# Kernel optimization log

Measured on AMD Instinct MI355X. Metric: run time of the kernel, lower is better.

Reference implementation:

```python
import jax, jax.numpy as jnp
import numpy as np

B, S, DIM = 2, 2048, 2048
QH, KVH = 32, 8
HD = DIM // QH            # 64
KV_DIM = HD * KVH         # 512
MAX_LEN = 2048
SCALE = HD ** -0.5
NEG_INF = -1e30


def _rope_cache(seq_len, head_dim, max_len, theta=10000.0, factor=8.0):
    # faithful to generate_sin_cos_pos_emb (causal branch, offset=0),
    # cache built at max_len then sliced to seq_len by the caller
    idx = np.arange(0, head_dim, 2, dtype=np.float64) / head_dim
    inv_freq = 1.0 / theta ** idx
    if factor > 1.0:
        seq_eff = max(max_len, max_len)  # generate called with seq_len=max_length
        adj = (factor * seq_eff / max_len - (factor - 1.0)) ** (head_dim / (head_dim - 2.0))
        inv_freq = 1.0 / (theta * adj) ** idx
    pos = np.arange(0, max_len, dtype=np.float64)
    freqs = np.einsum('i,j->ij', pos, inv_freq)
    emb = np.concatenate([freqs, freqs], axis=-1)  # [max_len, head_dim]
    cos = jnp.asarray(np.cos(emb)[:seq_len], dtype=jnp.float32)
    sin = jnp.asarray(np.sin(emb)[:seq_len], dtype=jnp.float32)
    return cos, sin


def _rotate_half(x):
    x1, x2 = jnp.split(x, 2, axis=-1)
    return jnp.concatenate([-x2, x1], axis=-1)


def _apply_rope(x, cos, sin):
    # x: [B, H, S, D]; cos/sin: [S, D]
    return x * cos + _rotate_half(x) * sin


def setup_inputs() -> dict:
    key = jax.random.key(0)
    ks = jax.random.split(key, 11)
    s = 0.02
    return {
        'query': jax.random.normal(ks[0], (B, S, DIM), jnp.float32),
        'key':   jax.random.normal(ks[1], (B, S, DIM), jnp.float32),
        'value': jax.random.normal(ks[2], (B, S, DIM), jnp.float32),
        'w_q': jax.random.normal(ks[3], (DIM, DIM), jnp.float32) * s,
        'b_q': jnp.zeros((DIM,), jnp.float32),
        'w_k': jax.random.normal(ks[4], (DIM, KV_DIM), jnp.float32) * s,
        'b_k': jnp.zeros((KV_DIM,), jnp.float32),
        'w_v': jax.random.normal(ks[5], (DIM, KV_DIM), jnp.float32) * s,
        'b_v': jnp.zeros((KV_DIM,), jnp.float32),
        'w_o': jax.random.normal(ks[6], (DIM, DIM), jnp.float32) * s,
        'b_o': jnp.zeros((DIM,), jnp.float32),
    }


def reference(query, key, value, w_q, b_q, w_k, b_k, w_v, b_v, w_o, b_o):
    # projections (weights stored as [in, out])
    q = query @ w_q + b_q                                    # [B,S,DIM]
    k = key   @ w_k + b_k                                    # [B,S,KV_DIM]
    v = value @ w_v + b_v                                    # [B,S,KV_DIM]

    q = q.reshape(B, S, QH, HD).transpose(0, 2, 1, 3)        # [B,QH,S,HD]
    k = k.reshape(B, S, KVH, HD).transpose(0, 2, 1, 3)       # [B,KVH,S,HD]
    v = v.reshape(B, S, KVH, HD).transpose(0, 2, 1, 3)       # [B,KVH,S,HD]

    cos, sin = _rope_cache(S, HD, MAX_LEN)
    q = _apply_rope(q, cos, sin)
    k = _apply_rope(k, cos, sin)

    # GQA: group queries per kv head (equivalent to repeat_interleave on K/V)
    G = QH // KVH
    qg = q.reshape(B, KVH, G, S, HD)
    scores = jnp.einsum('bhgqd,bhkd->bhgqk', qg, k) * SCALE  # [B,KVH,G,S,S]
    causal = jnp.tril(jnp.ones((S, S), dtype=bool))
    scores = jnp.where(causal, scores, NEG_INF)
    probs = jax.nn.softmax(scores, axis=-1)
    ctx = jnp.einsum('bhgqk,bhkd->bhgqd', probs, v)          # [B,KVH,G,S,HD]
    ctx = ctx.reshape(B, QH, S, HD).transpose(0, 2, 1, 3).reshape(B, S, DIM)
    return ctx @ w_o + b_o                                   # [B,S,DIM]
```

## Files before the change

kernel.cpp:

```cpp
#include <hip/hip_runtime.h>
#include <hip/hip_bf16.h>

typedef __hip_bfloat16 bf16_t;
typedef __attribute__((ext_vector_type(8))) short bf16x8;
typedef __attribute__((ext_vector_type(4))) float f32x4;

#define S_LEN   2048
#define D_MODEL 2048
#define N_QH    32
#define N_KVH   8
#define HEAD_D  64
#define KV_D    512
#define M_ROWS  4096
#define QK_SCALE (0.125f * 1.44269504088896340736f)
#define NQT     16

__global__ void rope_table_kernel(float* __restrict__ cosT, float* __restrict__ sinT) {
    int pos = blockIdx.x * 2 + (threadIdx.x >> 5);
    int j   = threadIdx.x & 31;
    double invf = pow(10000.0, -(double)(2 * j) / 64.0);
    double a = (double)pos * invf;
    cosT[pos * 32 + j] = (float)cos(a);
    sinT[pos * 32 + j] = (float)sin(a);
}

__global__ void wt_conv_all_kernel(const float* __restrict__ wq, const float* __restrict__ wk,
                                   const float* __restrict__ wv, const float* __restrict__ wo,
                                   bf16_t* __restrict__ tq, bf16_t* __restrict__ tk,
                                   bf16_t* __restrict__ tv, bf16_t* __restrict__ to) {
    __shared__ float tile[32][33];
    const int x = blockIdx.x;
    const float* W; bf16_t* Wt; int N, nb;
    if (x < 64)       { W = wq; Wt = tq; N = D_MODEL; nb = x; }
    else if (x < 80)  { W = wk; Wt = tk; N = KV_D;    nb = x - 64; }
    else if (x < 96)  { W = wv; Wt = tv; N = KV_D;    nb = x - 80; }
    else              { W = wo; Wt = to; N = D_MODEL; nb = x - 96; }
    const int K = D_MODEL;
    int n0 = nb * 32, k0 = blockIdx.y * 32;
    int tx = threadIdx.x & 31, ty = threadIdx.x >> 5;
#pragma unroll
    for (int i = 0; i < 4; i++) {
        int r = ty + i * 8;
        tile[r][tx] = W[(size_t)(k0 + r) * N + n0 + tx];
    }
    __syncthreads();
#pragma unroll
    for (int i = 0; i < 4; i++) {
        int r = ty + i * 8;
        Wt[(size_t)(n0 + r) * K + k0 + tx] = __float2bfloat16(tile[tx][r]);
    }
}

struct __align__(8) bf16x4s { bf16_t x, y, z, w; };

__device__ __forceinline__ void async_copy16(const bf16_t* g, bf16_t* l) {
    __builtin_amdgcn_global_load_lds((const __attribute__((address_space(1))) void*)g,
                                     (__attribute__((address_space(3))) void*)l, 16, 0, 0);
}

template <int ROPE, int OUTF32, int QSCALE>
__global__ __launch_bounds__(256, 2)
void gqa_gemm_kernel(const bf16_t* __restrict__ A, const bf16_t* __restrict__ Bt,
                     const float* __restrict__ bias, void* __restrict__ Cout,
                     int M, int N, int K,
                     const float* __restrict__ cosT, const float* __restrict__ sinT) {
    __shared__ __align__(16) bf16_t As[128 * 64];
    __shared__ __align__(16) bf16_t Bs[128 * 64];

    const int t = threadIdx.x;
    const int bx = blockIdx.x;
    const int xcd = bx & 7, j = bx >> 3;
    const int am0 = (((xcd >> 1) << 3) + (j >> 3)) * 128;
    const int bn0 = (((xcd & 1) << 3) + (j & 7)) * 128;

    const int l = t & 63, w = t >> 6;
    const int wr = w >> 1, wc = w & 1;
    const int lr = l & 15, lk = l >> 4;

    f32x4 acc[4][4];
#pragma unroll
    for (int i = 0; i < 4; i++)
#pragma unroll
        for (int jx = 0; jx < 4; jx++) acc[i][jx] = (f32x4)0.0f;

    const int r0 = t >> 3;
    const int c  = (t & 7) ^ (r0 & 7);
    const bf16_t* aptr = A + (size_t)(am0 + r0) * K + c * 8;
    const bf16_t* bptr = Bt + (size_t)(bn0 + r0) * K + c * 8;
    bf16_t* aLds = As + r0 * 64 + (t & 7) * 8;
    bf16_t* bLds = Bs + r0 * 64 + (t & 7) * 8;

    for (int k0 = 0; k0 < K; k0 += 64) {
#pragma unroll
        for (int s = 0; s < 4; ++s) {
            async_copy16(aptr + (size_t)(s * 32) * K + k0, aLds + s * 2048);
            async_copy16(bptr + (size_t)(s * 32) * K + k0, bLds + s * 2048);
        }
        __syncthreads();

        bf16x8 af[4][2], bfr[4][2];
#pragma unroll
        for (int mi = 0; mi < 4; mi++)
#pragma unroll
            for (int ks = 0; ks < 2; ks++)
                af[mi][ks] = *(const bf16x8*)&As[(wr * 64 + mi * 16 + lr) * 64 +
                                 ((ks * 32 + lk * 8) ^ ((lr & 7) << 3))];
#pragma unroll
        for (int ni = 0; ni < 4; ni++)
#pragma unroll
            for (int ks = 0; ks < 2; ks++)
                bfr[ni][ks] = *(const bf16x8*)&Bs[(wc * 64 + ni * 16 + lr) * 64 +
                                  ((ks * 32 + lk * 8) ^ ((lr & 7) << 3))];
#pragma unroll
        for (int mi = 0; mi < 4; mi++)
#pragma unroll
            for (int ni = 0; ni < 4; ni++)
#pragma unroll
                for (int ks = 0; ks < 2; ks++)
                    acc[mi][ni] = __builtin_amdgcn_mfma_f32_16x16x32_bf16(
                        af[mi][ks], bfr[ni][ks], acc[mi][ni], 0, 0, 0);
        __syncthreads();
    }

#pragma unroll
    for (int mi = 0; mi < 4; mi++) {
#pragma unroll
        for (int reg = 0; reg < 4; reg++) {
            int row = am0 + wr * 64 + mi * 16 + lk * 4 + reg;
            if (OUTF32) {
                float* out = (float*)Cout;
#pragma unroll
                for (int ni = 0; ni < 4; ni++) {
                    int col = bn0 + wc * 64 + ni * 16 + lr;
                    out[(size_t)row * N + col] = acc[mi][ni][reg] + bias[col];
                }
            } else if (ROPE) {
                bf16_t* out = (bf16_t*)Cout;
                int pos = row & (S_LEN - 1);
#pragma unroll
                for (int np = 0; np < 2; np++) {
                    int jj = np * 16 + lr;
                    float cs = cosT[pos * 32 + jj];
                    float sn = sinT[pos * 32 + jj];
                    int col1 = bn0 + wc * 64 + np * 16 + lr;
                    float x1 = acc[mi][np][reg] + bias[col1];
                    float x2 = acc[mi][np + 2][reg] + bias[col1 + 32];
                    float o1 = x1 * cs - x2 * sn;
                    float o2 = x2 * cs + x1 * sn;
                    if (QSCALE) { o1 *= QK_SCALE; o2 *= QK_SCALE; }
                    out[(size_t)row * N + col1]      = __float2bfloat16(o1);
                    out[(size_t)row * N + col1 + 32] = __float2bfloat16(o2);
                }
            } else {
                bf16_t* out = (bf16_t*)Cout;
#pragma unroll
                for (int ni = 0; ni < 4; ni++) {
                    int col = bn0 + wc * 64 + ni * 16 + lr;
                    out[(size_t)row * N + col] =
                        __float2bfloat16(acc[mi][ni][reg] + bias[col]);
                }
            }
        }
    }
}

__global__ __launch_bounds__(256, 4)
void gqa_kvc_kernel(const float* __restrict__ Key, const float* __restrict__ Val,
                    const float* __restrict__ Query,
                    const bf16_t* __restrict__ Wtk, const bf16_t* __restrict__ Wtv,
                    const float* __restrict__ bk, const float* __restrict__ bv,
                    bf16_t* __restrict__ Kout, bf16_t* __restrict__ VtOut,
                    bf16_t* __restrict__ Qbf,
                    const float* __restrict__ cosT, const float* __restrict__ sinT) {
    __shared__ __align__(16) char smem[9216];
    bf16_t* As  = (bf16_t*)smem;
    bf16_t* Bs  = (bf16_t*)(smem + 4096);
    bf16_t* VtE = (bf16_t*)smem;

    const int bx = blockIdx.x;
    const int t = threadIdx.x;

    if (bx >= 1024) {
        int tid = (bx - 1024) * 256 + t;
        const int total = M_ROWS * D_MODEL / 4;
#pragma unroll 4
        for (int i = tid; i < total; i += 512 * 256) {
            float4 v = ((const float4*)Query)[i];
            bf16x4s o;
            o.x = __float2bfloat16(v.x);
            o.y = __float2bfloat16(v.y);
            o.z = __float2bfloat16(v.z);
            o.w = __float2bfloat16(v.w);
            ((bf16x4s*)Qbf)[i] = o;
        }
        return;
    }

    constexpr int K = D_MODEL;
    const int xcd = bx & 7;
    const int j   = bx >> 3;
    const int z   = xcd >> 2;
    const int am0 = (((xcd & 3) << 4) + (j >> 3)) * 64;
    const int bn0 = (j & 7) * 64;

    const float* A32  = z ? Val : Key;
    const bf16_t* Bt  = z ? Wtv : Wtk;
    const float* bias = z ? bv : bk;

    const int l = t & 63, w = t >> 6;
    const int lr = l & 15, lk = l >> 4;

    f32x4 acc[4];
#pragma unroll
    for (int jx = 0; jx < 4; jx++) acc[jx] = (f32x4)0.0f;

    const int sr = t >> 2;
    const int sc = (t & 3) * 8;
    const float*  aptr = A32 + (size_t)(am0 + sr) * K + sc;
    const bf16_t* bptr = Bt + (size_t)(bn0 + sr) * K + sc;
    bf16_t* aLds = As + sr * 32 + sc;
    bf16_t* bLds = Bs + t * 8;

    float4 pa0 = ((const float4*)aptr)[0];
    float4 pa1 = ((const float4*)aptr)[1];

    for (int it = 0; it < K / 32; ++it) {
        union { bf16x8 v; bf16_t e[8]; } u;
        u.e[0] = __float2bfloat16(pa0.x); u.e[1] = __float2bfloat16(pa0.y);
        u.e[2] = __float2bfloat16(pa0.z); u.e[3] = __float2bfloat16(pa0.w);
        u.e[4] = __float2bfloat16(pa1.x); u.e[5] = __float2bfloat16(pa1.y);
        u.e[6] = __float2bfloat16(pa1.z); u.e[7] = __float2bfloat16(pa1.w);
        *(bf16x8*)aLds = u.v;
        async_copy16(bptr + it * 32, bLds);
        __builtin_amdgcn_sched_barrier(0);
        if (it + 1 < K / 32) {
            const float* ap = aptr + (it + 1) * 32;
            pa0 = ((const float4*)ap)[0];
            pa1 = ((const float4*)ap)[1];
            __builtin_amdgcn_sched_barrier(0);
            asm volatile("s_waitcnt lgkmcnt(0) vmcnt(2)" ::: "memory");
        } else {
            asm volatile("s_waitcnt lgkmcnt(0) vmcnt(0)" ::: "memory");
        }
        __builtin_amdgcn_sched_barrier(0);
        __builtin_amdgcn_s_barrier();
        __builtin_amdgcn_sched_barrier(0);

        bf16x8 af = *(const bf16x8*)&As[(w * 16 + lr) * 32 + lk * 8];
        bf16x8 bfr[4];
#pragma unroll
        for (int ni = 0; ni < 4; ni++)
            bfr[ni] = *(const bf16x8*)&Bs[(ni * 16 + lr) * 32 + lk * 8];
#pragma unroll
        for (int ni = 0; ni < 4; ni++)
            acc[ni] = __builtin_amdgcn_mfma_f32_16x16x32_bf16(af, bfr[ni], acc[ni], 0, 0, 0);
        __builtin_amdgcn_sched_barrier(0);
        __builtin_amdgcn_s_barrier();
        __builtin_amdgcn_sched_barrier(0);
    }

    if (z == 0) {
#pragma unroll
        for (int reg = 0; reg < 4; reg++) {
            int row = am0 + w * 16 + lk * 4 + reg;
            int pos = row & (S_LEN - 1);
#pragma unroll
            for (int np = 0; np < 2; np++) {
                int jj = np * 16 + lr;
                float cs = cosT[pos * 32 + jj];
                float sn = sinT[pos * 32 + jj];
                int col1 = bn0 + np * 16 + lr;
                float x1 = acc[np][reg] + bias[col1];
                float x2 = acc[np + 2][reg] + bias[col1 + 32];
                Kout[(size_t)row * KV_D + col1]      = __float2bfloat16(x1 * cs - x2 * sn);
                Kout[(size_t)row * KV_D + col1 + 32] = __float2bfloat16(x2 * cs + x1 * sn);
            }
        }
    } else {
        __syncthreads();
#pragma unroll
        for (int ni = 0; ni < 4; ni++) {
            bf16x4s pk;
            pk.x = __float2bfloat16(acc[ni][0] + bias[bn0 + ni * 16 + lr]);
            pk.y = __float2bfloat16(acc[ni][1] + bias[bn0 + ni * 16 + lr]);
            pk.z = __float2bfloat16(acc[ni][2] + bias[bn0 + ni * 16 + lr]);
            pk.w = __float2bfloat16(acc[ni][3] + bias[bn0 + ni * 16 + lr]);
            *(bf16x4s*)&VtE[(ni * 16 + lr) * 72 + w * 16 + lk * 4] = pk;
        }
        __syncthreads();
        const int d = t & 63, w2 = t >> 6;
        const int bI = am0 >> 11;
        const int kvhI = bn0 >> 6;
        const int sl = (am0 & (S_LEN - 1)) + w2 * 16;
        bf16_t* dst = VtOut + ((size_t)(bI * N_KVH + kvhI) * HEAD_D + d) * S_LEN + sl;
        const bf16_t* src = &VtE[d * 72 + w2 * 16];
        *(bf16x8*)dst       = *(const bf16x8*)src;
        *(bf16x8*)(dst + 8) = *(const bf16x8*)(src + 8);
    }
}

__device__ __forceinline__ void stage_K8(const bf16_t* KB, bf16_t* dst, int kt, int t) {
    const int skey = t >> 3;
    const int c    = (t & 7) ^ (skey & 7);
    async_copy16(KB + (size_t)(kt * 64 + skey) * KV_D + c * 8, dst + t * 8);
}
__device__ __forceinline__ void stage_V8(const bf16_t* VTb, bf16_t* dst, int kt, int t) {
    const int sd = t >> 3;
    const int c  = (t & 7) ^ (sd & 7);
    async_copy16(VTb + (size_t)sd * S_LEN + kt * 64 + c * 8, dst + t * 8);
}

__global__ __launch_bounds__(512, 4)
void gqa_attn_kernel(const bf16_t* __restrict__ Q, const bf16_t* __restrict__ Kb,
                     const bf16_t* __restrict__ VT, bf16_t* __restrict__ Ctx) {
    __shared__ __align__(16) bf16_t Ks[2][64 * 64];
    __shared__ __align__(16) bf16_t Vs[2][64 * 64];
    __shared__ __align__(16) bf16_t Pw[8][16 * 72];

    const int t = threadIdx.x, l = t & 63, w = t >> 6;
    const int lr = l & 15, lk = l >> 4;

    const int flat = blockIdx.x;
    const int xcd = flat & 7, j0 = flat >> 3;
    const int combo  = xcd * 2 + (j0 >> 5);
    const int within = j0 & 31;
    const int b   = combo >> 3;
    const int kvh = combo & 7;
    const int h   = kvh * 4 + (within >> 3);
    const int p   = within & 7;

    const bf16_t* KB  = Kb + (size_t)b * S_LEN * KV_D + kvh * HEAD_D;
    const bf16_t* VTb = VT + ((size_t)(b * N_KVH + kvh) * HEAD_D) * S_LEN;

#pragma unroll
    for (int half = 0; half < 2; ++half) {
        const int qt  = half ? (NQT - 1 - p) : p;
        const int q0w = qt * 128 + w * 16;
        const int qg  = q0w + lr;

        bf16x8 qf[2];
        {
            const bf16_t* qrow = Q + ((size_t)(b * S_LEN + qg)) * D_MODEL + h * HEAD_D;
            qf[0] = *(const bf16x8*)(qrow + lk * 8);
            qf[1] = *(const bf16x8*)(qrow + 32 + lk * 8);
        }

        float lrow = 0.f;
        f32x4 oaccT[4];
#pragma unroll
        for (int df = 0; df < 4; df++) oaccT[df] = (f32x4)0.0f;

        const int nkt = 2 * qt + 2;

        stage_K8(KB, Ks[0], 0, t);
        stage_V8(VTb, Vs[0], 0, t);
        __syncthreads();

        int cur = 0;
        for (int kt = 0; kt < nkt; ++kt) {
            const bool pre = (kt + 1 < nkt);
            if (pre) {
                stage_K8(KB, Ks[cur ^ 1], kt + 1, t);
                stage_V8(VTb, Vs[cur ^ 1], kt + 1, t);
            }

            if (kt * 64 <= q0w + 15) {
                const bool diag = (kt * 64 + 63 > q0w);

                f32x4 sfrT[4];
#pragma unroll
                for (int ni = 0; ni < 4; ni++) sfrT[ni] = (f32x4)0.0f;
                __builtin_amdgcn_s_setprio(1);
#pragma unroll
                for (int ni = 0; ni < 4; ni++)
#pragma unroll
                    for (int ks = 0; ks < 2; ks++) {
                        bf16x8 kf = *(const bf16x8*)&Ks[cur][(ni * 16 + lr) * 64 +
                                        ((ks * 32 + lk * 8) ^ ((lr & 7) << 3))];
                        sfrT[ni] = __builtin_amdgcn_mfma_f32_16x16x32_bf16(kf, qf[ks],
                                                                           sfrT[ni], 0, 0, 0);
                    }
                __builtin_amdgcn_s_setprio(0);

                float rsp[4] = {0.f, 0.f, 0.f, 0.f};
                float pe[16];
#pragma unroll
                for (int ni = 0; ni < 4; ni++)
#pragma unroll
                    for (int r = 0; r < 4; r++) {
                        float sc = sfrT[ni][r];
                        if (diag) {
                            int keyg = kt * 64 + ni * 16 + lk * 4 + r;
                            if (keyg > qg) sc = -1e30f;
                        }
                        float e = exp2f(sc);
                        pe[ni * 4 + r] = e;
                        rsp[ni] += e;
                    }
                float rs = (rsp[0] + rsp[1]) + (rsp[2] + rsp[3]);
                rs += __shfl_xor(rs, 16);
                rs += __shfl_xor(rs, 32);
                lrow += rs;

#pragma unroll
                for (int ni = 0; ni < 4; ni++) {
                    bf16x4s pk;
                    pk.x = __float2bfloat16(pe[ni * 4 + 0]);
                    pk.y = __float2bfloat16(pe[ni * 4 + 1]);
                    pk.z = __float2bfloat16(pe[ni * 4 + 2]);
                    pk.w = __float2bfloat16(pe[ni * 4 + 3]);
                    *(bf16x4s*)&Pw[w][lr * 72 + ni * 16 + lk * 4] = pk;
                }

                __builtin_amdgcn_s_setprio(1);
#pragma unroll
                for (int ks = 0; ks < 2; ks++) {
                    bf16x8 pf = *(const bf16x8*)&Pw[w][lr * 72 + ks * 32 + lk * 8];
#pragma unroll
                    for (int df = 0; df < 4; df++) {
                        bf16x8 vf = *(const bf16x8*)&Vs[cur][(df * 16 + lr) * 64 +
                                        ((ks * 32 + lk * 8) ^ ((lr & 7) << 3))];
                        oaccT[df] = __builtin_amdgcn_mfma_f32_16x16x32_bf16(vf, pf,
                                            oaccT[df], 0, 0, 0);
                    }
                }
                __builtin_amdgcn_s_setprio(0);
            }

            __syncthreads();
            cur ^= 1;
        }

        {
            float inv = 1.0f / lrow;
            bf16_t* crow = Ctx + ((size_t)(b * S_LEN + qg)) * D_MODEL + h * HEAD_D;
#pragma unroll
            for (int df = 0; df < 4; df++) {
                bf16x4s ov;
                ov.x = __float2bfloat16(oaccT[df][0] * inv);
                ov.y = __float2bfloat16(oaccT[df][1] * inv);
                ov.z = __float2bfloat16(oaccT[df][2] * inv);
                ov.w = __float2bfloat16(oaccT[df][3] * inv);
                *(bf16x4s*)(crow + df * 16 + lk * 4) = ov;
            }
        }
    }
}

extern "C" void kernel_launch(void* const* d_in, const int* in_sizes, int n_in,
                              void* d_out, int out_size, void* d_ws, size_t ws_size,
                              hipStream_t stream) {
    const float* query = (const float*)d_in[0];
    const float* key_  = (const float*)d_in[1];
    const float* value = (const float*)d_in[2];
    const float* w_q = (const float*)d_in[3];
    const float* b_q = (const float*)d_in[4];
    const float* w_k = (const float*)d_in[5];
    const float* b_k = (const float*)d_in[6];
    const float* w_v = (const float*)d_in[7];
    const float* b_v = (const float*)d_in[8];
    const float* w_o = (const float*)d_in[9];
    const float* b_o = (const float*)d_in[10];
    float* out = (float*)d_out;

    char* ws = (char*)d_ws;
    bf16_t* Abuf = (bf16_t*)(ws);
    bf16_t* qb   = (bf16_t*)(ws + (size_t)(16 << 20));
    bf16_t* kb   = (bf16_t*)(ws + (size_t)(32 << 20));
    bf16_t* vt   = (bf16_t*)(ws + (size_t)(36 << 20));
    bf16_t* wtq  = (bf16_t*)(ws + (size_t)(40 << 20));
    bf16_t* wtk  = (bf16_t*)(ws + (size_t)(48 << 20));
    bf16_t* wtv  = (bf16_t*)(ws + (size_t)(50 << 20));
    bf16_t* wto  = (bf16_t*)(ws + (size_t)(52 << 20));
    float* cosT  = (float*)(ws + (size_t)(60 << 20));
    float* sinT  = (float*)(ws + (size_t)(60 << 20) + (256 << 10));

    rope_table_kernel<<<S_LEN / 2, 64, 0, stream>>>(cosT, sinT);

    wt_conv_all_kernel<<<dim3(160, 64), 256, 0, stream>>>(w_q, w_k, w_v, w_o,
                                                          wtq, wtk, wtv, wto);

    gqa_kvc_kernel<<<1536, 256, 0, stream>>>(key_, value, query, wtk, wtv,
                                             b_k, b_v, kb, vt, Abuf, cosT, sinT);

    gqa_gemm_kernel<1, 0, 1><<<512, 256, 0, stream>>>(
        Abuf, wtq, b_q, qb, M_ROWS, D_MODEL, D_MODEL, cosT, sinT);

    gqa_attn_kernel<<<512, 512, 0, stream>>>(qb, kb, vt, Abuf);

    gqa_gemm_kernel<0, 1, 0><<<512, 256, 0, stream>>>(
        Abuf, wto, b_o, out, M_ROWS, D_MODEL, D_MODEL, cosT, sinT);
}
```

Before: 215.5 us.

## Fuse Q projection into KV projection kernel and compute softmax denominator via MFMA

The rope table generation moves into an extra block column of the weight-conversion kernel, and the Q projection GEMM (with bias, RoPE and scale) now runs in the same launch as the K/V projections. It reads fp32 query directly instead of first writing a bf16 copy. This removes two kernel launches and a full query conversion pass. In attention, the per-row exp sum is accumulated with an extra MFMA against a ones vector instead of shuffles, which trades a little matrix work for fewer VALU/shuffle ops. The Q path uses a 64x128 tile with one wave per 16 rows, which may lower its efficiency compared with the dedicated GEMM kernel.

```diff
diff --git a/kernel.cpp b/kernel.cpp
--- a/kernel.cpp
+++ b/kernel.cpp
@@ -15,21 +15,25 @@
 #define QK_SCALE (0.125f * 1.44269504088896340736f)
 #define NQT     16
 
-__global__ void rope_table_kernel(float* __restrict__ cosT, float* __restrict__ sinT) {
-    int pos = blockIdx.x * 2 + (threadIdx.x >> 5);
-    int j   = threadIdx.x & 31;
-    double invf = pow(10000.0, -(double)(2 * j) / 64.0);
-    double a = (double)pos * invf;
-    cosT[pos * 32 + j] = (float)cos(a);
-    sinT[pos * 32 + j] = (float)sin(a);
-}
-
 __global__ void wt_conv_all_kernel(const float* __restrict__ wq, const float* __restrict__ wk,
                                    const float* __restrict__ wv, const float* __restrict__ wo,
                                    bf16_t* __restrict__ tq, bf16_t* __restrict__ tk,
-                                   bf16_t* __restrict__ tv, bf16_t* __restrict__ to) {
+                                   bf16_t* __restrict__ tv, bf16_t* __restrict__ to,
+                                   float* __restrict__ cosT, float* __restrict__ sinT) {
+    const int x = blockIdx.x;
+    if (x == 160) {
+        int j = threadIdx.x & 31;
+        double invf = pow(10000.0, -(double)(2 * j) / 64.0);
+#pragma unroll
+        for (int i = 0; i < 4; i++) {
+            int pos = blockIdx.y * 32 + i * 8 + (threadIdx.x >> 5);
+            double a = (double)pos * invf;
+            cosT[pos * 32 + j] = (float)cos(a);
+            sinT[pos * 32 + j] = (float)sin(a);
+        }
+        return;
+    }
     __shared__ float tile[32][33];
-    const int x = blockIdx.x;
     const float* W; bf16_t* Wt; int N, nb;
     if (x < 64)       { W = wq; Wt = tq; N = D_MODEL; nb = x; }
     else if (x < 80)  { W = wk; Wt = tk; N = KV_D;    nb = x - 64; }
@@ -165,38 +169,104 @@
 }
 
 __global__ __launch_bounds__(256, 4)
-void gqa_kvc_kernel(const float* __restrict__ Key, const float* __restrict__ Val,
+void gqa_kvq_kernel(const float* __restrict__ Key, const float* __restrict__ Val,
                     const float* __restrict__ Query,
                     const bf16_t* __restrict__ Wtk, const bf16_t* __restrict__ Wtv,
+                    const bf16_t* __restrict__ Wtq,
                     const float* __restrict__ bk, const float* __restrict__ bv,
+                    const float* __restrict__ bq,
                     bf16_t* __restrict__ Kout, bf16_t* __restrict__ VtOut,
-                    bf16_t* __restrict__ Qbf,
+                    bf16_t* __restrict__ Qout,
                     const float* __restrict__ cosT, const float* __restrict__ sinT) {
-    __shared__ __align__(16) char smem[9216];
+    __shared__ __align__(16) char smem[12288];
     bf16_t* As  = (bf16_t*)smem;
     bf16_t* Bs  = (bf16_t*)(smem + 4096);
     bf16_t* VtE = (bf16_t*)smem;
 
     const int bx = blockIdx.x;
     const int t = threadIdx.x;
+    const int l = t & 63, w = t >> 6;
+    const int lr = l & 15, lk = l >> 4;
+    const int sr = t >> 2;
+    const int sc = (t & 3) * 8;
+    constexpr int K = D_MODEL;
 
     if (bx >= 1024) {
-        int tid = (bx - 1024) * 256 + t;
-        const int total = M_ROWS * D_MODEL / 4;
-#pragma unroll 4
-        for (int i = tid; i < total; i += 512 * 256) {
-            float4 v = ((const float4*)Query)[i];
-            bf16x4s o;
-            o.x = __float2bfloat16(v.x);
-            o.y = __float2bfloat16(v.y);
-            o.z = __float2bfloat16(v.z);
-            o.w = __float2bfloat16(v.w);
-            ((bf16x4s*)Qbf)[i] = o;
+        const int qbx = bx - 1024;
+        const int xcd = qbx & 7;
+        const int j   = qbx >> 3;
+        const int am0 = ((xcd << 3) + (j & 7)) * 64;
+        const int bn0 = (j >> 3) * 128;
+
+        f32x4 acc[8];
+#pragma unroll
+        for (int jx = 0; jx < 8; jx++) acc[jx] = (f32x4)0.0f;
+
+        const float*  aptr = Query + (size_t)(am0 + sr) * K + sc;
+        const bf16_t* bptr = Wtq + (size_t)(bn0 + sr) * K + sc;
+        bf16_t* aLds  = As + sr * 32 + sc;
+        bf16_t* bLds  = Bs + t * 8;
+
+        float4 pa0 = ((const float4*)aptr)[0];
+        float4 pa1 = ((const float4*)aptr)[1];
+
+        for (int it = 0; it < K / 32; ++it) {
+            union { bf16x8 v; bf16_t e[8]; } u;
+            u.e[0] = __float2bfloat16(pa0.x); u.e[1] = __float2bfloat16(pa0.y);
+            u.e[2] = __float2bfloat16(pa0.z); u.e[3] = __float2bfloat16(pa0.w);
+            u.e[4] = __float2bfloat16(pa1.x); u.e[5] = __float2bfloat16(pa1.y);
+            u.e[6] = __float2bfloat16(pa1.z); u.e[7] = __float2bfloat16(pa1.w);
+            *(bf16x8*)aLds = u.v;
+            async_copy16(bptr + it * 32, bLds);
+            async_copy16(bptr + (size_t)64 * K + it * 32, bLds + 2048);
+            __builtin_amdgcn_sched_barrier(0);
+            if (it + 1 < K / 32) {
+                const float* ap = aptr + (it + 1) * 32;
+                pa0 = ((const float4*)ap)[0];
+                pa1 = ((const float4*)ap)[1];
+                __builtin_amdgcn_sched_barrier(0);
+                asm volatile("s_waitcnt lgkmcnt(0) vmcnt(2)" ::: "memory");
+            } else {
+                asm volatile("s_waitcnt lgkmcnt(0) vmcnt(0)" ::: "memory");
+            }
+            __builtin_amdgcn_sched_barrier(0);
+            __builtin_amdgcn_s_barrier();
+            __builtin_amdgcn_sched_barrier(0);
+
+            bf16x8 af = *(const bf16x8*)&As[(w * 16 + lr) * 32 + lk * 8];
+#pragma unroll
+            for (int ni = 0; ni < 8; ni++) {
+                bf16x8 bfr = *(const bf16x8*)&Bs[(ni * 16 + lr) * 32 + lk * 8];
+                acc[ni] = __builtin_amdgcn_mfma_f32_16x16x32_bf16(af, bfr, acc[ni], 0, 0, 0);
+            }
+            __builtin_amdgcn_sched_barrier(0);
+            __builtin_amdgcn_s_barrier();
+            __builtin_amdgcn_sched_barrier(0);
+        }
+
+#pragma unroll
+        for (int reg = 0; reg < 4; reg++) {
+            int row = am0 + w * 16 + lk * 4 + reg;
+            int pos = row & (S_LEN - 1);
+#pragma unroll
+            for (int hg = 0; hg < 2; hg++)
+#pragma unroll
+                for (int np = 0; np < 2; np++) {
+                    int jj = np * 16 + lr;
+                    float cs = cosT[pos * 32 + jj];
+                    float sn = sinT[pos * 32 + jj];
+                    int col1 = bn0 + hg * 64 + np * 16 + lr;
+                    float x1 = acc[hg * 4 + np][reg] + bq[col1];
+                    float x2 = acc[hg * 4 + np + 2][reg] + bq[col1 + 32];
+                    Qout[(size_t)row * D_MODEL + col1] =
+                        __float2bfloat16((x1 * cs - x2 * sn) * QK_SCALE);
+                    Qout[(size_t)row * D_MODEL + col1 + 32] =
+                        __float2bfloat16((x2 * cs + x1 * sn) * QK_SCALE);
+                }
         }
         return;
     }
 
-    constexpr int K = D_MODEL;
     const int xcd = bx & 7;
     const int j   = bx >> 3;
     const int z   = xcd >> 2;
@@ -207,15 +277,10 @@
     const bf16_t* Bt  = z ? Wtv : Wtk;
     const float* bias = z ? bv : bk;
 
-    const int l = t & 63, w = t >> 6;
-    const int lr = l & 15, lk = l >> 4;
-
     f32x4 acc[4];
 #pragma unroll
     for (int jx = 0; jx < 4; jx++) acc[jx] = (f32x4)0.0f;
 
-    const int sr = t >> 2;
-    const int sc = (t & 3) * 8;
     const float*  aptr = A32 + (size_t)(am0 + sr) * K + sc;
     const bf16_t* bptr = Bt + (size_t)(bn0 + sr) * K + sc;
     bf16_t* aLds = As + sr * 32 + sc;
@@ -247,13 +312,11 @@
         __builtin_amdgcn_sched_barrier(0);
 
         bf16x8 af = *(const bf16x8*)&As[(w * 16 + lr) * 32 + lk * 8];
-        bf16x8 bfr[4];
-#pragma unroll
-        for (int ni = 0; ni < 4; ni++)
-            bfr[ni] = *(const bf16x8*)&Bs[(ni * 16 + lr) * 32 + lk * 8];
-#pragma unroll
-        for (int ni = 0; ni < 4; ni++)
-            acc[ni] = __builtin_amdgcn_mfma_f32_16x16x32_bf16(af, bfr[ni], acc[ni], 0, 0, 0);
+#pragma unroll
+        for (int ni = 0; ni < 4; ni++) {
+            bf16x8 bfr = *(const bf16x8*)&Bs[(ni * 16 + lr) * 32 + lk * 8];
+            acc[ni] = __builtin_amdgcn_mfma_f32_16x16x32_bf16(af, bfr, acc[ni], 0, 0, 0);
+        }
         __builtin_amdgcn_sched_barrier(0);
         __builtin_amdgcn_s_barrier();
         __builtin_amdgcn_sched_barrier(0);
@@ -329,6 +392,10 @@
     const int h   = kvh * 4 + (within >> 3);
     const int p   = within & 7;
 
+    bf16x8 vones;
+#pragma unroll
+    for (int i = 0; i < 8; i++) vones[i] = (short)0x3F80;
+
     const bf16_t* KB  = Kb + (size_t)b * S_LEN * KV_D + kvh * HEAD_D;
     const bf16_t* VTb = VT + ((size_t)(b * N_KVH + kvh) * HEAD_D) * S_LEN;
 
@@ -345,8 +412,8 @@
             qf[1] = *(const bf16x8*)(qrow + 32 + lk * 8);
         }
 
-        float lrow = 0.f;
         f32x4 oaccT[4];
+        f32x4 oaccS = (f32x4)0.0f;
 #pragma unroll
         for (int df = 0; df < 4; df++) oaccT[df] = (f32x4)0.0f;
 
@@ -382,33 +449,27 @@
                     }
                 __builtin_amdgcn_s_setprio(0);
 
-                float rsp[4] = {0.f, 0.f, 0.f, 0.f};
-                float pe[16];
-#pragma unroll
-                for (int ni = 0; ni < 4; ni++)
-#pragma unroll
-                    for (int r = 0; r < 4; r++) {
-                        float sc = sfrT[ni][r];
+#pragma unroll
+                for (int ni = 0; ni < 4; ni++) {
+                    float e0, e1, e2, e3;
+                    {
+                        float sc0 = sfrT[ni][0], sc1 = sfrT[ni][1];
+                        float sc2 = sfrT[ni][2], sc3 = sfrT[ni][3];
                         if (diag) {
-                            int keyg = kt * 64 + ni * 16 + lk * 4 + r;
-                            if (keyg > qg) sc = -1e30f;
+                            int kbase = kt * 64 + ni * 16 + lk * 4;
+                            if (kbase + 0 > qg) sc0 = -1e30f;
+                            if (kbase + 1 > qg) sc1 = -1e30f;
+                            if (kbase + 2 > qg) sc2 = -1e30f;
+                            if (kbase + 3 > qg) sc3 = -1e30f;
                         }
-                        float e = exp2f(sc);
-                        pe[ni * 4 + r] = e;
-                        rsp[ni] += e;
+                        e0 = exp2f(sc0); e1 = exp2f(sc1);
+                        e2 = exp2f(sc2); e3 = exp2f(sc3);
                     }
-                float rs = (rsp[0] + rsp[1]) + (rsp[2] + rsp[3]);
-                rs += __shfl_xor(rs, 16);
-                rs += __shfl_xor(rs, 32);
-                lrow += rs;
-
-#pragma unroll
-                for (int ni = 0; ni < 4; ni++) {
                     bf16x4s pk;
-                    pk.x = __float2bfloat16(pe[ni * 4 + 0]);
-                    pk.y = __float2bfloat16(pe[ni * 4 + 1]);
-                    pk.z = __float2bfloat16(pe[ni * 4 + 2]);
-                    pk.w = __float2bfloat16(pe[ni * 4 + 3]);
+                    pk.x = __float2bfloat16(e0);
+                    pk.y = __float2bfloat16(e1);
+                    pk.z = __float2bfloat16(e2);
+                    pk.w = __float2bfloat16(e3);
                     *(bf16x4s*)&Pw[w][lr * 72 + ni * 16 + lk * 4] = pk;
                 }
 
@@ -416,6 +477,7 @@
 #pragma unroll
                 for (int ks = 0; ks < 2; ks++) {
                     bf16x8 pf = *(const bf16x8*)&Pw[w][lr * 72 + ks * 32 + lk * 8];
+                    oaccS = __builtin_amdgcn_mfma_f32_16x16x32_bf16(vones, pf, oaccS, 0, 0, 0);
 #pragma unroll
                     for (int df = 0; df < 4; df++) {
                         bf16x8 vf = *(const bf16x8*)&Vs[cur][(df * 16 + lr) * 64 +
@@ -432,7 +494,7 @@
         }
 
         {
-            float inv = 1.0f / lrow;
+            float inv = 1.0f / oaccS[0];
             bf16_t* crow = Ctx + ((size_t)(b * S_LEN + qg)) * D_MODEL + h * HEAD_D;
 #pragma unroll
             for (int df = 0; df < 4; df++) {
@@ -475,16 +537,11 @@
     float* cosT  = (float*)(ws + (size_t)(60 << 20));
     float* sinT  = (float*)(ws + (size_t)(60 << 20) + (256 << 10));
 
-    rope_table_kernel<<<S_LEN / 2, 64, 0, stream>>>(cosT, sinT);
-
-    wt_conv_all_kernel<<<dim3(160, 64), 256, 0, stream>>>(w_q, w_k, w_v, w_o,
-                                                          wtq, wtk, wtv, wto);
-
-    gqa_kvc_kernel<<<1536, 256, 0, stream>>>(key_, value, query, wtk, wtv,
-                                             b_k, b_v, kb, vt, Abuf, cosT, sinT);
-
-    gqa_gemm_kernel<1, 0, 1><<<512, 256, 0, stream>>>(
-        Abuf, wtq, b_q, qb, M_ROWS, D_MODEL, D_MODEL, cosT, sinT);
+    wt_conv_all_kernel<<<dim3(161, 64), 256, 0, stream>>>(w_q, w_k, w_v, w_o,
+                                                          wtq, wtk, wtv, wto, cosT, sinT);
+
+    gqa_kvq_kernel<<<2048, 256, 0, stream>>>(key_, value, query, wtk, wtv, wtq,
+                                             b_k, b_v, b_q, kb, vt, qb, cosT, sinT);
 
     gqa_attn_kernel<<<512, 512, 0, stream>>>(qb, kb, vt, Abuf);
 
```

After: 224.9 us. 1.04x slower.

## Fuse RoPE table into weight conversion; compute softmax row sums via MFMA

Applied to the files above, without the earlier changes.

Removes the separate RoPE table launch by giving the weight-transpose kernel an extra column of blocks that fills the cos/sin tables, saving one kernel launch. In attention, the per-row sum of exponentials is no longer built with VALU adds and cross-lane shuffles. It is computed by an extra MFMA that multiplies the bf16 probability tile by a vector of ones. That trades shuffle and add work for one more matrix instruction per k-step. The denominator now sums bf16-rounded probabilities, which matches the numerator more closely but changes the numerics slightly.

```diff
diff --git a/kernel.cpp b/kernel.cpp
--- a/kernel.cpp
+++ b/kernel.cpp
@@ -15,21 +15,25 @@
 #define QK_SCALE (0.125f * 1.44269504088896340736f)
 #define NQT     16
 
-__global__ void rope_table_kernel(float* __restrict__ cosT, float* __restrict__ sinT) {
-    int pos = blockIdx.x * 2 + (threadIdx.x >> 5);
-    int j   = threadIdx.x & 31;
-    double invf = pow(10000.0, -(double)(2 * j) / 64.0);
-    double a = (double)pos * invf;
-    cosT[pos * 32 + j] = (float)cos(a);
-    sinT[pos * 32 + j] = (float)sin(a);
-}
-
 __global__ void wt_conv_all_kernel(const float* __restrict__ wq, const float* __restrict__ wk,
                                    const float* __restrict__ wv, const float* __restrict__ wo,
                                    bf16_t* __restrict__ tq, bf16_t* __restrict__ tk,
-                                   bf16_t* __restrict__ tv, bf16_t* __restrict__ to) {
+                                   bf16_t* __restrict__ tv, bf16_t* __restrict__ to,
+                                   float* __restrict__ cosT, float* __restrict__ sinT) {
+    const int x = blockIdx.x;
+    if (x == 160) {
+        int j = threadIdx.x & 31;
+        double invf = pow(10000.0, -(double)(2 * j) / 64.0);
+#pragma unroll
+        for (int i = 0; i < 4; i++) {
+            int pos = blockIdx.y * 32 + i * 8 + (threadIdx.x >> 5);
+            double a = (double)pos * invf;
+            cosT[pos * 32 + j] = (float)cos(a);
+            sinT[pos * 32 + j] = (float)sin(a);
+        }
+        return;
+    }
     __shared__ float tile[32][33];
-    const int x = blockIdx.x;
     const float* W; bf16_t* Wt; int N, nb;
     if (x < 64)       { W = wq; Wt = tq; N = D_MODEL; nb = x; }
     else if (x < 80)  { W = wk; Wt = tk; N = KV_D;    nb = x - 64; }
@@ -329,6 +333,10 @@
     const int h   = kvh * 4 + (within >> 3);
     const int p   = within & 7;
 
+    bf16x8 vones;
+#pragma unroll
+    for (int i = 0; i < 8; i++) vones[i] = (short)0x3F80;
+
     const bf16_t* KB  = Kb + (size_t)b * S_LEN * KV_D + kvh * HEAD_D;
     const bf16_t* VTb = VT + ((size_t)(b * N_KVH + kvh) * HEAD_D) * S_LEN;
 
@@ -345,8 +353,8 @@
             qf[1] = *(const bf16x8*)(qrow + 32 + lk * 8);
         }
 
-        float lrow = 0.f;
         f32x4 oaccT[4];
+        f32x4 oaccS = (f32x4)0.0f;
 #pragma unroll
         for (int df = 0; df < 4; df++) oaccT[df] = (f32x4)0.0f;
 
@@ -382,33 +390,22 @@
                     }
                 __builtin_amdgcn_s_setprio(0);
 
-                float rsp[4] = {0.f, 0.f, 0.f, 0.f};
-                float pe[16];
-#pragma unroll
-                for (int ni = 0; ni < 4; ni++)
-#pragma unroll
-                    for (int r = 0; r < 4; r++) {
-                        float sc = sfrT[ni][r];
-                        if (diag) {
-                            int keyg = kt * 64 + ni * 16 + lk * 4 + r;
-                            if (keyg > qg) sc = -1e30f;
-                        }
-                        float e = exp2f(sc);
-                        pe[ni * 4 + r] = e;
-                        rsp[ni] += e;
+#pragma unroll
+                for (int ni = 0; ni < 4; ni++) {
+                    float sc0 = sfrT[ni][0], sc1 = sfrT[ni][1];
+                    float sc2 = sfrT[ni][2], sc3 = sfrT[ni][3];
+                    if (diag) {
+                        int kbase = kt * 64 + ni * 16 + lk * 4;
+                        if (kbase + 0 > qg) sc0 = -1e30f;
+                        if (kbase + 1 > qg) sc1 = -1e30f;
+                        if (kbase + 2 > qg) sc2 = -1e30f;
+                        if (kbase + 3 > qg) sc3 = -1e30f;
                     }
-                float rs = (rsp[0] + rsp[1]) + (rsp[2] + rsp[3]);
-                rs += __shfl_xor(rs, 16);
-                rs += __shfl_xor(rs, 32);
-                lrow += rs;
-
-#pragma unroll
-                for (int ni = 0; ni < 4; ni++) {
                     bf16x4s pk;
-                    pk.x = __float2bfloat16(pe[ni * 4 + 0]);
-                    pk.y = __float2bfloat16(pe[ni * 4 + 1]);
-                    pk.z = __float2bfloat16(pe[ni * 4 + 2]);
-                    pk.w = __float2bfloat16(pe[ni * 4 + 3]);
+                    pk.x = __float2bfloat16(exp2f(sc0));
+                    pk.y = __float2bfloat16(exp2f(sc1));
+                    pk.z = __float2bfloat16(exp2f(sc2));
+                    pk.w = __float2bfloat16(exp2f(sc3));
                     *(bf16x4s*)&Pw[w][lr * 72 + ni * 16 + lk * 4] = pk;
                 }
 
@@ -416,6 +413,7 @@
 #pragma unroll
                 for (int ks = 0; ks < 2; ks++) {
                     bf16x8 pf = *(const bf16x8*)&Pw[w][lr * 72 + ks * 32 + lk * 8];
+                    oaccS = __builtin_amdgcn_mfma_f32_16x16x32_bf16(vones, pf, oaccS, 0, 0, 0);
 #pragma unroll
                     for (int df = 0; df < 4; df++) {
                         bf16x8 vf = *(const bf16x8*)&Vs[cur][(df * 16 + lr) * 64 +
@@ -432,7 +430,7 @@
         }
 
         {
-            float inv = 1.0f / lrow;
+            float inv = 1.0f / oaccS[0];
             bf16_t* crow = Ctx + ((size_t)(b * S_LEN + qg)) * D_MODEL + h * HEAD_D;
 #pragma unroll
             for (int df = 0; df < 4; df++) {
@@ -475,10 +473,8 @@
     float* cosT  = (float*)(ws + (size_t)(60 << 20));
     float* sinT  = (float*)(ws + (size_t)(60 << 20) + (256 << 10));
 
-    rope_table_kernel<<<S_LEN / 2, 64, 0, stream>>>(cosT, sinT);
-
-    wt_conv_all_kernel<<<dim3(160, 64), 256, 0, stream>>>(w_q, w_k, w_v, w_o,
-                                                          wtq, wtk, wtv, wto);
+    wt_conv_all_kernel<<<dim3(161, 64), 256, 0, stream>>>(w_q, w_k, w_v, w_o,
+                                                          wtq, wtk, wtv, wto, cosT, sinT);
 
     gqa_kvc_kernel<<<1536, 256, 0, stream>>>(key_, value, query, wtk, wtv,
                                              b_k, b_v, kb, vt, Abuf, cosT, sinT);
```

Result: faster. 211.2 us (-2.0%).
